# Kernel tuning notes

Measured on AMD Instinct MI355X. Metric: run time of the kernel, lower is better.

The kernel has to match this reference:

```python
import jax, jax.numpy as jnp
import numpy as np

B, L, D = 4096, 64, 128
NUM_IDS = 1000


def setup_inputs() -> dict:
    key = jax.random.key(0)
    ks = jax.random.split(key, 8)
    src_node_ids = jax.random.randint(ks[0], (B,), 0, NUM_IDS, dtype=jnp.int32)
    dst_node_ids = jax.random.randint(ks[1], (B,), 0, NUM_IDS, dtype=jnp.int32)
    src_nb = jax.random.randint(ks[2], (B, L), 0, NUM_IDS, dtype=jnp.int32)
    dst_nb = jax.random.randint(ks[3], (B, L), 0, NUM_IDS, dtype=jnp.int32)
    # MLP params: Linear(1 -> D), ReLU, Linear(D -> D)
    W1 = jax.random.normal(ks[4], (1, D), dtype=jnp.float32) / jnp.sqrt(1.0)
    b1 = jnp.zeros((D,), dtype=jnp.float32)
    W2 = jax.random.normal(ks[5], (D, D), dtype=jnp.float32) / jnp.sqrt(D)
    b2 = jnp.zeros((D,), dtype=jnp.float32)
    return {
        "src_node_ids": src_node_ids,
        "dst_node_ids": dst_node_ids,
        "src_nodes_neighbor_ids": src_nb,
        "dst_nodes_neighbor_ids": dst_nb,
        "W1": W1, "b1": b1, "W2": W2, "b2": b2,
    }


def _appearances(src_id, dst_id, src_nb, dst_nb):
    # counts of each neighbor within its own list: (B, L)
    c_src = (src_nb[:, :, None] == src_nb[:, None, :]).sum(-1)
    c_dst = (dst_nb[:, :, None] == dst_nb[:, None, :]).sum(-1)
    # cross counts: count of src neighbor in dst list and vice versa
    c_dst_of_src = (src_nb[:, :, None] == dst_nb[:, None, :]).sum(-1)  # (B, L)
    c_src_of_dst = (dst_nb[:, :, None] == src_nb[:, None, :]).sum(-1)  # (B, L)
    # scalar per batch: count of src_id in dst list, dst_id in src list
    cd_srcid = (dst_nb == src_id[:, None]).sum(-1)  # (B,)
    cs_dstid = (src_nb == dst_id[:, None]).sum(-1)  # (B,)
    srcid_in_dst = cd_srcid > 0
    same = src_id == dst_id
    # dict-mutation semantics of count_nodes_appearances:
    # src_mapping[src_id] overwritten with cd_srcid when src_id in dst list
    # dst_mapping[dst_id] overwritten with (post-mutation) src_mapping[dst_id]
    cond2 = (cs_dstid > 0) | (same & srcid_in_dst)
    v2 = jnp.where(same & srcid_in_dst, cd_srcid, cs_dstid)
    # dst_mapping.get(src neighbors): count in dst, with dst_id override
    src_col1 = jnp.where((src_nb == dst_id[:, None]) & cond2[:, None],
                         v2[:, None], c_dst_of_src)
    # src_mapping.get(dst neighbors): count in src, with src_id override
    dst_col0 = jnp.where((dst_nb == src_id[:, None]) & srcid_in_dst[:, None],
                         cd_srcid[:, None], c_src_of_dst)
    src_app = jnp.stack([c_src, src_col1], axis=-1).astype(jnp.float32)  # (B,L,2)
    dst_app = jnp.stack([dst_col0, c_dst], axis=-1).astype(jnp.float32)  # (B,L,2)
    return src_app, dst_app


def _mlp(app, W1, b1, W2, b2):
    # app: (B, L, 2) -> (B, L, 2, D) -> sum over the 2 co-occurrence channels
    h = jax.nn.relu(app[..., None] * W1[0] + b1)      # (B, L, 2, D)
    out = jnp.einsum('blcd,de->blce', h, W2) + b2     # (B, L, 2, D)
    return out.sum(axis=2)                            # (B, L, D)


def reference(src_node_ids, dst_node_ids, src_nodes_neighbor_ids,
              dst_nodes_neighbor_ids, W1, b1, W2, b2):
    src_app, dst_app = _appearances(src_node_ids, dst_node_ids,
                                    src_nodes_neighbor_ids, dst_nodes_neighbor_ids)
    src_feat = _mlp(src_app, W1, b1, W2, b2)
    dst_feat = _mlp(dst_app, W1, b1, W2, b2)
    return src_feat, dst_feat
```

## Files before the change

kernel.cpp:

```cpp
#include <hip/hip_runtime.h>

#define DD   128
#define LLEN 64
#define TMAX 65
#define ROWS_PER_BLK 4
#define TAB4 (TMAX * (DD / 4))

typedef __attribute__((ext_vector_type(4))) float f32x4;

__global__ void build_table_kernel(const float* __restrict__ W1,
                                   const float* __restrict__ b1,
                                   const float* __restrict__ W2,
                                   const float* __restrict__ b2,
                                   float* __restrict__ tab) {
    const int a = blockIdx.x;
    const int e = threadIdx.x;
    const float fa = (float)a;
    float acc = b2[e];
#pragma unroll 8
    for (int d = 0; d < DD; ++d) {
        float h = fmaxf(fmaf(fa, W1[d], b1[d]), 0.f);
        acc = fmaf(h, W2[d * DD + e], acc);
    }
    tab[a * DD + e] = acc;
}

__global__ __launch_bounds__(256, 4) void nif_main_kernel(
    const int* __restrict__ src_id, const int* __restrict__ dst_id,
    const int* __restrict__ src_nb, const int* __restrict__ dst_nb,
    const float* __restrict__ tab, float* __restrict__ out, int B) {
    __shared__ f32x4 TAB[TAB4];

    const int tid  = threadIdx.x;
    const int lane = tid & 63;
    const int w    = tid >> 6;
    const int b    = blockIdx.x * ROWS_PER_BLK + w;

    const int vs  = src_nb[(size_t)b * LLEN + lane];
    const int vd  = dst_nb[(size_t)b * LLEN + lane];
    const int sid = src_id[b];
    const int did = dst_id[b];

    const f32x4* __restrict__ tabg = (const f32x4*)tab;
#pragma unroll
    for (int i = 0; i < 8; ++i) TAB[tid + 256 * i] = tabg[tid + 256 * i];
    if (tid < TAB4 - 2048) TAB[2048 + tid] = tabg[2048 + tid];

    int c_src = 0, c_dos = 0, c_dst = 0, c_sod = 0;
#pragma unroll 8
    for (int j = 0; j < LLEN; ++j) {
        const int sj = __shfl(vs, j);
        const int dj = __shfl(vd, j);
        c_src += (sj == vs);
        c_dos += (dj == vs);
        c_dst += (dj == vd);
        c_sod += (sj == vd);
    }
    const int cd_sid = __popcll(__ballot(vd == sid));
    const int cs_did = __popcll(__ballot(vs == did));
    const bool s_in_d = (cd_sid > 0);
    const bool same   = (sid == did);
    const bool c2     = (cs_did > 0) || (same && s_in_d);
    const int  v2     = (same && s_in_d) ? cd_sid : cs_did;
    const int A0 = c_src;
    const int A1 = (vs == did && c2) ? v2 : c_dos;
    const int C0 = (vd == sid && s_in_d) ? cd_sid : c_sod;
    const int C1 = c_dst;

    __syncthreads();

    const int e4 = lane & 31;
    const int lh = lane >> 5;
    const size_t src_base = (size_t)b * (LLEN * DD / 4);
    const size_t dst_base = src_base + (size_t)B * (LLEN * DD / 4);
    f32x4* __restrict__ myout =
        (f32x4*)out + (lh ? dst_base : src_base) + e4;

#pragma unroll 4
    for (int l = 0; l < LLEN; ++l) {
        const int a0 = __shfl(A0, l);
        const int a1 = __shfl(A1, l);
        const int c0 = __shfl(C0, l);
        const int c1 = __shfl(C1, l);
        const int p = lh ? c0 : a0;
        const int q = lh ? c1 : a1;
        const f32x4 t = TAB[p * 32 + e4] + TAB[q * 32 + e4];
        __builtin_nontemporal_store(t, myout + (size_t)l * 32);
    }
}

extern "C" void kernel_launch(void* const* d_in, const int* in_sizes, int n_in,
                              void* d_out, int out_size, void* d_ws, size_t ws_size,
                              hipStream_t stream) {
    const int*   src_id = (const int*)d_in[0];
    const int*   dst_id = (const int*)d_in[1];
    const int*   src_nb = (const int*)d_in[2];
    const int*   dst_nb = (const int*)d_in[3];
    const float* W1     = (const float*)d_in[4];
    const float* b1     = (const float*)d_in[5];
    const float* W2     = (const float*)d_in[6];
    const float* b2     = (const float*)d_in[7];
    float*       out    = (float*)d_out;
    float*       tab    = (float*)d_ws;

    const int B = in_sizes[0];

    build_table_kernel<<<TMAX, DD, 0, stream>>>(W1, b1, W2, b2, tab);
    nif_main_kernel<<<B / ROWS_PER_BLK, 256, 0, stream>>>(
        src_id, dst_id, src_nb, dst_nb, tab, out, B);
}
```

Baseline: 290.2 us.

## Split count computation and output store into separate kernels with packed indices

Splits the fused kernel in two. The first kernel computes the co-occurrence counts and packs the four 8-bit indices into one word per neighbor in a workspace buffer. The second is a persistent grid-stride kernel with 1024 blocks. Each block loads the lookup table into LDS once, then writes fully contiguous 1 KB chunks per wave using regular stores instead of nontemporal ones. This spreads the LDS table-load cost over more output and gives a streaming write pattern, at the cost of an extra launch and an index round-trip through global memory.

Measured after the change: 295.5 us. No clear change (+1.8%).

```diff
diff --git a/kernel.cpp b/kernel.cpp
--- a/kernel.cpp
+++ b/kernel.cpp
@@ -3,7 +3,6 @@
 #define DD   128
 #define LLEN 64
 #define TMAX 65
-#define ROWS_PER_BLK 4
 #define TAB4 (TMAX * (DD / 4))
 
 typedef __attribute__((ext_vector_type(4))) float f32x4;
@@ -25,26 +24,19 @@
     tab[a * DD + e] = acc;
 }
 
-__global__ __launch_bounds__(256, 4) void nif_main_kernel(
+__global__ __launch_bounds__(256) void build_index_kernel(
     const int* __restrict__ src_id, const int* __restrict__ dst_id,
     const int* __restrict__ src_nb, const int* __restrict__ dst_nb,
-    const float* __restrict__ tab, float* __restrict__ out, int B) {
-    __shared__ f32x4 TAB[TAB4];
-
+    unsigned* __restrict__ IDX, int B) {
     const int tid  = threadIdx.x;
     const int lane = tid & 63;
     const int w    = tid >> 6;
-    const int b    = blockIdx.x * ROWS_PER_BLK + w;
+    const int b    = blockIdx.x * 4 + w;
 
     const int vs  = src_nb[(size_t)b * LLEN + lane];
     const int vd  = dst_nb[(size_t)b * LLEN + lane];
     const int sid = src_id[b];
     const int did = dst_id[b];
-
-    const f32x4* __restrict__ tabg = (const f32x4*)tab;
-#pragma unroll
-    for (int i = 0; i < 8; ++i) TAB[tid + 256 * i] = tabg[tid + 256 * i];
-    if (tid < TAB4 - 2048) TAB[2048 + tid] = tabg[2048 + tid];
 
     int c_src = 0, c_dos = 0, c_dst = 0, c_sod = 0;
 #pragma unroll 8
@@ -62,30 +54,49 @@
     const bool same   = (sid == did);
     const bool c2     = (cs_did > 0) || (same && s_in_d);
     const int  v2     = (same && s_in_d) ? cd_sid : cs_did;
-    const int A0 = c_src;
-    const int A1 = (vs == did && c2) ? v2 : c_dos;
-    const int C0 = (vd == sid && s_in_d) ? cd_sid : c_sod;
-    const int C1 = c_dst;
+    const unsigned A0 = c_src;
+    const unsigned A1 = (vs == did && c2) ? v2 : c_dos;
+    const unsigned C0 = (vd == sid && s_in_d) ? cd_sid : c_sod;
+    const unsigned C1 = c_dst;
 
+    IDX[(size_t)b * LLEN + lane] = A0 | (A1 << 8) | (C0 << 16) | (C1 << 24);
+}
+
+__global__ __launch_bounds__(256) void nif_store_kernel(
+    const float* __restrict__ tab, const unsigned* __restrict__ IDX,
+    float* __restrict__ out, int B) {
+    __shared__ f32x4 TAB[TAB4];
+
+    const int tid  = threadIdx.x;
+    const int lane = tid & 63;
+    const int w    = tid >> 6;
+    const int e4   = lane & 31;
+    const int lh   = lane >> 5;
+
+    const f32x4* __restrict__ tabg = (const f32x4*)tab;
+#pragma unroll
+    for (int i = 0; i < 8; ++i) TAB[tid + 256 * i] = tabg[tid + 256 * i];
+    if (tid < TAB4 - 2048) TAB[2048 + tid] = tabg[2048 + tid];
     __syncthreads();
 
-    const int e4 = lane & 31;
-    const int lh = lane >> 5;
-    const size_t src_base = (size_t)b * (LLEN * DD / 4);
-    const size_t dst_base = src_base + (size_t)B * (LLEN * DD / 4);
-    f32x4* __restrict__ myout =
-        (f32x4*)out + (lh ? dst_base : src_base) + e4;
+    const int NSRC = B * (LLEN / 2);
+    const int NCH  = B * LLEN;
+    const int gw     = blockIdx.x * 4 + w;
+    const int stride = gridDim.x * 4;
+
+    f32x4* __restrict__ out4 = (f32x4*)out;
 
 #pragma unroll 4
-    for (int l = 0; l < LLEN; ++l) {
-        const int a0 = __shfl(A0, l);
-        const int a1 = __shfl(A1, l);
-        const int c0 = __shfl(C0, l);
-        const int c1 = __shfl(C1, l);
-        const int p = lh ? c0 : a0;
-        const int q = lh ? c1 : a1;
+    for (int g = gw; g < NCH; g += stride) {
+        const bool isdst = (g >= NSRC);
+        const int  gc    = isdst ? g - NSRC : g;
+        const unsigned row0u = __builtin_amdgcn_readfirstlane(2 * gc);
+        const uint2 xx = *(const uint2*)(IDX + row0u);
+        const unsigned x = lh ? xx.y : xx.x;
+        const int p = isdst ? (int)((x >> 16) & 255) : (int)(x & 255);
+        const int q = isdst ? (int)((x >> 24) & 255) : (int)((x >> 8) & 255);
         const f32x4 t = TAB[p * 32 + e4] + TAB[q * 32 + e4];
-        __builtin_nontemporal_store(t, myout + (size_t)l * 32);
+        out4[(size_t)g * 64 + lane] = t;
     }
 }
 
@@ -102,10 +113,12 @@
     const float* b2     = (const float*)d_in[7];
     float*       out    = (float*)d_out;
     float*       tab    = (float*)d_ws;
+    unsigned*    IDX    = (unsigned*)((char*)d_ws + 65536);
 
     const int B = in_sizes[0];
 
     build_table_kernel<<<TMAX, DD, 0, stream>>>(W1, b1, W2, b2, tab);
-    nif_main_kernel<<<B / ROWS_PER_BLK, 256, 0, stream>>>(
-        src_id, dst_id, src_nb, dst_nb, tab, out, B);
+    build_index_kernel<<<B / 4, 256, 0, stream>>>(
+        src_id, dst_id, src_nb, dst_nb, IDX, B);
+    nif_store_kernel<<<1024, 256, 0, stream>>>(tab, IDX, out, B);
 }
```
